# Kernel tuning notes

Hardware: AMD Instinct MI355X
Metric: run time of the kernel (lower is better)

Reference implementation:

```python
import jax, jax.numpy as jnp
import numpy as np

EPS = 1e-5
NUM_HEADS = 8

def layernorm(x, g, b):
    m = x.mean(-1, keepdims=True)
    v = ((x - m) ** 2).mean(-1, keepdims=True)
    return (x - m) / jnp.sqrt(v + EPS) * g + b

def mha(x, qkv_w, qkv_b, proj_w, proj_b):
    # x: [B, N, C]; weights stored [in, out] (transposed torch Linear)
    B, N, C = x.shape
    hd = C // NUM_HEADS
    scale = hd ** -0.5
    qkv = (x @ qkv_w + qkv_b).reshape(B, N, 3, NUM_HEADS, hd)
    qkv = jnp.transpose(qkv, (2, 0, 3, 1, 4))  # [3, B, H, N, hd]
    q, k, v = qkv[0], qkv[1], qkv[2]
    attn = jax.nn.softmax(jnp.einsum('bhnd,bhmd->bhnm', q, k) * scale, axis=-1)
    o = jnp.einsum('bhnm,bhmd->bhnd', attn, v)
    o = jnp.transpose(o, (0, 2, 1, 3)).reshape(B, N, C)
    return o @ proj_w + proj_b

def gelu(x):
    return jax.nn.gelu(x, approximate=False)

def setup_inputs() -> dict:
    key = jax.random.key(0)
    C, H = 512, 2048
    B, P, NI = 2, 196, 16
    N = 1 + NI * P
    ks = jax.random.split(key, 16)
    s = 0.02
    d = {
        'x': jax.random.normal(ks[0], (B, N, C), jnp.float32),
        'num_patches_per_image': P,
        'ln1_g': jnp.ones((C,)), 'ln1_b': jnp.zeros((C,)),
        'ln2_g': jnp.ones((C,)), 'ln2_b': jnp.zeros((C,)),
        'ln3_g': jnp.ones((C,)), 'ln3_b': jnp.zeros((C,)),
        'g_qkv_w': jax.random.normal(ks[1], (C, 3 * C)) * s,
        'g_qkv_b': jnp.zeros((3 * C,)),
        'g_proj_w': jax.random.normal(ks[2], (C, C)) * s,
        'g_proj_b': jnp.zeros((C,)),
        'l_qkv_w': jax.random.normal(ks[3], (C, 3 * C)) * s,
        'l_qkv_b': jnp.zeros((3 * C,)),
        'l_proj_w': jax.random.normal(ks[4], (C, C)) * s,
        'l_proj_b': jnp.zeros((C,)),
        'mlp_w1': jax.random.normal(ks[5], (C, H)) * s,
        'mlp_b1': jnp.zeros((H,)),
        'mlp_w2': jax.random.normal(ks[6], (H, C)) * s,
        'mlp_b2': jnp.zeros((C,)),
    }
    return d

def reference(x, num_patches_per_image, ln1_g, ln1_b, ln2_g, ln2_b, ln3_g, ln3_b,
              g_qkv_w, g_qkv_b, g_proj_w, g_proj_b,
              l_qkv_w, l_qkv_b, l_proj_w, l_proj_b,
              mlp_w1, mlp_b1, mlp_w2, mlp_b2):
    B, N, C = x.shape
    P = int(num_patches_per_image)
    NI = (N - 1) // P
    # global attention over all tokens (incl. CLS)
    x = x + mha(layernorm(x, ln1_g, ln1_b), g_qkv_w, g_qkv_b, g_proj_w, g_proj_b)
    cls_tok = x[:, 0:1, :]
    patches = x[:, 1:, :]
    # local attention: block-diagonal per-image mask == independent attention
    # within each image block (masked entries underflow to exactly 0 in softmax)
    pn = layernorm(patches, ln2_g, ln2_b).reshape(B * NI, P, C)
    local = mha(pn, l_qkv_w, l_qkv_b, l_proj_w, l_proj_b).reshape(B, NI * P, C)
    patches = patches + local
    x = jnp.concatenate([cls_tok, patches], axis=1)
    h = layernorm(x, ln3_g, ln3_b)
    h = gelu(h @ mlp_w1 + mlp_b1) @ mlp_w2 + mlp_b2
    return x + h
```

## Files before the change

### kernel.cpp

```cpp
#include <hip/hip_runtime.h>
#include <math.h>

typedef __attribute__((ext_vector_type(8))) short bf16x8;
typedef __attribute__((ext_vector_type(4))) short bf16x4_t;
typedef __attribute__((ext_vector_type(4))) float f32x4;
typedef __attribute__((ext_vector_type(4))) unsigned int u32x4;

typedef const __attribute__((address_space(1))) unsigned int glb_u32;
typedef __attribute__((address_space(3))) unsigned int lds_u32;
#define GLOAD_LDS16(g, l) __builtin_amdgcn_global_load_lds( \
    (glb_u32*)(const void*)(g), (lds_u32*)(void*)(l), 16, 0, 0)

static __device__ __forceinline__ float4 ld4(const float* p) {
    return *reinterpret_cast<const float4*>(p);
}
static __device__ __forceinline__ unsigned short f2bf(float f) {
    unsigned int u = __float_as_uint(f);
    u += 0x7fffu + ((u >> 16) & 1u);
    return (unsigned short)(u >> 16);
}

__global__ __launch_bounds__(64) void ln_kernel(
    const float* __restrict__ in, const float* __restrict__ g,
    const float* __restrict__ bta, unsigned short* __restrict__ out, int mode)
{
    int r = blockIdx.x;
    int lane = threadIdx.x;
    int in_r = mode ? (r + 1 + r / 3136) : r;
    const float* xp = in + (size_t)in_r * 512 + lane * 8;
    float4 v0 = ld4(xp), v1 = ld4(xp + 4);
    float s  = v0.x + v0.y + v0.z + v0.w + v1.x + v1.y + v1.z + v1.w;
    float sq = v0.x*v0.x + v0.y*v0.y + v0.z*v0.z + v0.w*v0.w
             + v1.x*v1.x + v1.y*v1.y + v1.z*v1.z + v1.w*v1.w;
    #pragma unroll
    for (int off = 32; off; off >>= 1) {
        s  += __shfl_xor(s, off);
        sq += __shfl_xor(sq, off);
    }
    float mean = s * (1.f / 512.f);
    float var  = fmaxf(sq * (1.f / 512.f) - mean * mean, 0.f);
    float rstd = rsqrtf(var + 1e-5f);
    float4 g0 = ld4(g + lane * 8),   g1 = ld4(g + lane * 8 + 4);
    float4 b0 = ld4(bta + lane * 8), b1 = ld4(bta + lane * 8 + 4);
    float o0 = (v0.x - mean) * rstd * g0.x + b0.x;
    float o1 = (v0.y - mean) * rstd * g0.y + b0.y;
    float o2 = (v0.z - mean) * rstd * g0.z + b0.z;
    float o3 = (v0.w - mean) * rstd * g0.w + b0.w;
    float o4 = (v1.x - mean) * rstd * g1.x + b1.x;
    float o5 = (v1.y - mean) * rstd * g1.y + b1.y;
    float o6 = (v1.z - mean) * rstd * g1.z + b1.z;
    float o7 = (v1.w - mean) * rstd * g1.w + b1.w;
    u32x4 pk;
    pk[0] = (unsigned int)f2bf(o0) | ((unsigned int)f2bf(o1) << 16);
    pk[1] = (unsigned int)f2bf(o2) | ((unsigned int)f2bf(o3) << 16);
    pk[2] = (unsigned int)f2bf(o4) | ((unsigned int)f2bf(o5) << 16);
    pk[3] = (unsigned int)f2bf(o6) | ((unsigned int)f2bf(o7) << 16);
    *(u32x4*)(out + (size_t)r * 512 + lane * 8) = pk;
}

struct TransArgs {
    const float* src[6];
    unsigned short* dst[6];
    int N[6], K[6], off[6];
};

__global__ __launch_bounds__(256) void transpose_all(TransArgs a)
{
    __shared__ unsigned short tile[32][34];
    int t = blockIdx.x;
    int i = 0;
    #pragma unroll
    for (int j = 1; j < 6; ++j) if (t >= a.off[j]) i = j;
    int rel = t - a.off[i];
    int tx_n = a.N[i] >> 5;
    int bx = (rel % tx_n) * 32, by = (rel / tx_n) * 32;
    const float* W = a.src[i];
    unsigned short* WT = a.dst[i];
    int K = a.K[i], N = a.N[i];
    int tx = threadIdx.x & 31, ty = threadIdx.x >> 5;
    #pragma unroll
    for (int r = 0; r < 32; r += 8)
        tile[ty + r][tx] = f2bf(W[(size_t)(by + ty + r) * N + bx + tx]);
    __syncthreads();
    #pragma unroll
    for (int r = 0; r < 32; r += 8)
        WT[(size_t)(bx + ty + r) * K + by + tx] = tile[tx][ty + r];
}

template<int BM, int BN, int OUT_BF16>
__global__ __launch_bounds__(256) void mfma_gemm(
    const unsigned short* __restrict__ A, const unsigned short* __restrict__ WT,
    const float* __restrict__ bias, const float* __restrict__ resid,
    void* __restrict__ outp, int M, int N, int K,
    int rowmap, int act,
    unsigned short* __restrict__ vt_out,
    int vtNs, unsigned int vtMagic, int vtNsP, int vtColBase)
{
    constexpr int FI = BM / 32, FJ = BN / 32;
    constexpr int AL = BM / 64, BL = BN / 64;
    __shared__ __align__(16) unsigned short As[2][BM * 32];
    __shared__ __align__(16) unsigned short Bs[2][BN * 32];

    int tid = threadIdx.x;
    int m0 = blockIdx.x * BM, n0 = blockIdx.y * BN;
    int w = tid >> 6, l = tid & 63;
    int wm = (w >> 1) * (BM / 2), wn = (w & 1) * (BN / 2);
    int lr = l & 15, lg = l >> 4;

    int lrow = l >> 2;
    int lcol = (l & 3) * 8;

    f32x4 zero = {0.f, 0.f, 0.f, 0.f};
    f32x4 acc[FI][FJ];
    #pragma unroll
    for (int i = 0; i < FI; ++i)
        #pragma unroll
        for (int j = 0; j < FJ; ++j) acc[i][j] = zero;

#define STAGE(buf, kk) do { \
    _Pragma("unroll") \
    for (int q = 0; q < AL; ++q) { \
        int rb = (w * AL + q) * 16; \
        GLOAD_LDS16(A + (size_t)(m0 + rb + lrow) * K + (kk) + lcol, \
                    &As[buf][rb * 32]); \
    } \
    _Pragma("unroll") \
    for (int q = 0; q < BL; ++q) { \
        int rb = (w * BL + q) * 16; \
        GLOAD_LDS16(WT + (size_t)(n0 + rb + lrow) * K + (kk) + lcol, \
                    &Bs[buf][rb * 32]); \
    } \
} while (0)

    int nk = K >> 5;
    STAGE(0, 0);
    STAGE(1, 32);
    for (int s = 0; s < nk; ++s) {
        int cur = s & 1;
        if (s + 1 < nk) {
            if constexpr (AL + BL == 2)
                asm volatile("s_waitcnt vmcnt(2)" ::: "memory");
            else if constexpr (AL + BL == 3)
                asm volatile("s_waitcnt vmcnt(3)" ::: "memory");
            else
                asm volatile("s_waitcnt vmcnt(4)" ::: "memory");
        } else {
            asm volatile("s_waitcnt vmcnt(0)" ::: "memory");
        }
        __builtin_amdgcn_s_barrier();

        bf16x8 af[FI], bfr[FJ];
        #pragma unroll
        for (int i = 0; i < FI; ++i)
            af[i] = *(const bf16x8*)&As[cur][(wm + i * 16 + lr) * 32 + lg * 8];
        #pragma unroll
        for (int j = 0; j < FJ; ++j)
            bfr[j] = *(const bf16x8*)&Bs[cur][(wn + j * 16 + lr) * 32 + lg * 8];
        asm volatile("s_waitcnt lgkmcnt(0)" ::: "memory");
        __builtin_amdgcn_sched_barrier(0);
        __builtin_amdgcn_s_barrier();
        if (s + 2 < nk) STAGE(cur, (s + 2) * 32);

        #pragma unroll
        for (int i = 0; i < FI; ++i)
            #pragma unroll
            for (int j = 0; j < FJ; ++j)
                acc[i][j] = __builtin_amdgcn_mfma_f32_16x16x32_bf16(
                    af[i], bfr[j], acc[i][j], 0, 0, 0);
    }
#undef STAGE

    int rowW = vt_out ? vtColBase : N;
    #pragma unroll
    for (int i = 0; i < FI; ++i) {
        #pragma unroll
        for (int r = 0; r < 4; ++r) {
            int row = m0 + wm + i * 16 + lg * 4 + r;
            if (row >= M) continue;
            int orow = rowmap ? (row + 1 + row / 3136) : row;
            #pragma unroll
            for (int j = 0; j < FJ; ++j) {
                int col = n0 + wn + j * 16 + lr;
                if (col >= N) continue;
                float v = acc[i][j][r] + bias[col];
                if (act) v = 0.5f * v * (1.f + erff(v * 0.70710678118654752f));
                if (resid) v += resid[(size_t)orow * N + col];
                if (vt_out && col >= vtColBase) {
                    unsigned int bb = (unsigned int)(((unsigned long long)(unsigned int)row * vtMagic) >> 32);
                    int nn = row - (int)bb * vtNs;
                    vt_out[((size_t)bb * 512 + (col - vtColBase)) * vtNsP + nn] = f2bf(v);
                } else if (OUT_BF16) {
                    ((unsigned short*)outp)[(size_t)orow * rowW + col] = f2bf(v);
                } else {
                    ((float*)outp)[(size_t)orow * rowW + col] = v;
                }
            }
        }
    }
}

__global__ __launch_bounds__(256) void attn_mfma(
    const unsigned short* __restrict__ qk, const unsigned short* __restrict__ vT,
    unsigned short* __restrict__ o, int Ns, int NsP)
{
    __shared__ __align__(16) unsigned short Ks[64 * 64];
    __shared__ __align__(16) unsigned short VsT[64 * 72];

    int tid = threadIdx.x;
    int h = blockIdx.y, b = blockIdx.z;
    int mb = b * Ns;
    int l = tid & 63, w = tid >> 6;
    int g = l >> 4, c16 = l & 15;

    int qrow = blockIdx.x * 64 + w * 16 + c16;
    int qr = (qrow < Ns ? qrow : Ns - 1) + mb;
    const unsigned short* qp = qk + (size_t)qr * 1024 + h * 64;
    bf16x8 bQ0 = *(const bf16x8*)(qp + g * 8);
    bf16x8 bQ1 = *(const bf16x8*)(qp + 32 + g * 8);

    f32x4 zero = {0.f, 0.f, 0.f, 0.f};
    f32x4 Oacc[4] = {zero, zero, zero, zero};
    float mrun = -1e30f, lrun = 0.f;

    int sk = tid >> 2, sc0 = tid & 3;
    int kswz = (sk & 7) ^ (sk >> 3);
    int kdst0 = sk * 64 + ((sc0 ^ kswz) * 8);
    int kdst1 = sk * 64 + (((sc0 + 4) ^ kswz) * 8);
    int vdst0 = sk * 72 + sc0 * 8;
    int vdst1 = sk * 72 + (sc0 + 4) * 8;
    const unsigned short* kbase = qk + (size_t)mb * 1024 + 512 + h * 64;
    const unsigned short* vrow = vT + ((size_t)b * 512 + h * 64 + sk) * NsP;

    int ka[4][2];
    #pragma unroll
    for (int f = 0; f < 4; ++f) {
        int key = 16 * f + c16;
        int swz = (key & 7) ^ (key >> 3);
        ka[f][0] = key * 64 + ((g ^ swz) * 8);
        ka[f][1] = key * 64 + (((4 + g) ^ swz) * 8);
    }

    const float SCL = 0.125f * 1.4426950408889634f;
    int nt = (Ns + 63) >> 6;
    int tail = Ns & 63;

    u32x4 kv0, kv1, vv0, vv1;
    {
        int kr = sk < Ns ? sk : Ns - 1;
        const unsigned short* kp = kbase + (size_t)kr * 1024;
        kv0 = *(const u32x4*)(kp + sc0 * 8);
        kv1 = *(const u32x4*)(kp + (sc0 + 4) * 8);
        vv0 = *(const u32x4*)(vrow + sc0 * 8);
        vv1 = *(const u32x4*)(vrow + (sc0 + 4) * 8);
    }

    for (int kt = 0; kt < nt; ++kt) {
        __syncthreads();
        *(u32x4*)&Ks[kdst0] = kv0;
        *(u32x4*)&Ks[kdst1] = kv1;
        *(u32x4*)&VsT[vdst0] = vv0;
        *(u32x4*)&VsT[vdst1] = vv1;
        __syncthreads();

        if (kt + 1 < nt) {
            int kr = (kt + 1) * 64 + sk; if (kr >= Ns) kr = Ns - 1;
            const unsigned short* kp = kbase + (size_t)kr * 1024;
            kv0 = *(const u32x4*)(kp + sc0 * 8);
            kv1 = *(const u32x4*)(kp + (sc0 + 4) * 8);
            int kb = (kt + 1) * 64;
            vv0 = *(const u32x4*)(vrow + kb + sc0 * 8);
            vv1 = *(const u32x4*)(vrow + kb + (sc0 + 4) * 8);
        }

        f32x4 st[4];
        #pragma unroll
        for (int f = 0; f < 4; ++f) {
            bf16x8 a0 = *(const bf16x8*)&Ks[ka[f][0]];
            bf16x8 a1 = *(const bf16x8*)&Ks[ka[f][1]];
            f32x4 a = zero;
            a = __builtin_amdgcn_mfma_f32_16x16x32_bf16(a0, bQ0, a, 0, 0, 0);
            a = __builtin_amdgcn_mfma_f32_16x16x32_bf16(a1, bQ1, a, 0, 0, 0);
            st[f] = a;
        }

        float sv[16];
        #pragma unroll
        for (int f = 0; f < 4; ++f)
            #pragma unroll
            for (int r = 0; r < 4; ++r) sv[4 * f + r] = st[f][r];
        if (kt == nt - 1 && tail) {
            #pragma unroll
            for (int f = 0; f < 4; ++f)
                #pragma unroll
                for (int r = 0; r < 4; ++r)
                    if (16 * f + 4 * g + r >= tail) sv[4 * f + r] = -1e30f;
        }
        float mloc = sv[0];
        #pragma unroll
        for (int e = 1; e < 16; ++e) mloc = fmaxf(mloc, sv[e]);
        if (!__all(mloc - mrun <= 64.f)) {
            mloc = fmaxf(mloc, __shfl_xor(mloc, 16));
            mloc = fmaxf(mloc, __shfl_xor(mloc, 32));
            float mnew = fmaxf(mrun, mloc);
            float sc = exp2f((mrun - mnew) * SCL);
            lrun *= sc;
            #pragma unroll
            for (int j = 0; j < 4; ++j) {
                Oacc[j][0] *= sc; Oacc[j][1] *= sc;
                Oacc[j][2] *= sc; Oacc[j][3] *= sc;
            }
            mrun = mnew;
        }
        float nl = mrun * SCL;
        #pragma unroll
        for (int e = 0; e < 16; ++e) {
            sv[e] = exp2f(fmaf(sv[e], SCL, -nl));
            lrun += sv[e];
        }

        union { unsigned int u[4]; bf16x8 v; } plo, phi;
        #pragma unroll
        for (int wi = 0; wi < 4; ++wi) {
            asm("v_cvt_pk_bf16_f32 %0, %1, %2"
                : "=v"(plo.u[wi]) : "v"(sv[2 * wi]), "v"(sv[2 * wi + 1]));
            asm("v_cvt_pk_bf16_f32 %0, %1, %2"
                : "=v"(phi.u[wi]) : "v"(sv[8 + 2 * wi]), "v"(sv[8 + 2 * wi + 1]));
        }

        #pragma unroll
        for (int j = 0; j < 4; ++j) {
            int vb = (16 * j + c16) * 72 + 4 * g;
            bf16x4_t t0 = *(const bf16x4_t*)&VsT[vb];
            bf16x4_t t1 = *(const bf16x4_t*)&VsT[vb + 16];
            bf16x4_t t2 = *(const bf16x4_t*)&VsT[vb + 32];
            bf16x4_t t3 = *(const bf16x4_t*)&VsT[vb + 48];
            bf16x8 aVlo = __builtin_shufflevector(t0, t1, 0, 1, 2, 3, 4, 5, 6, 7);
            bf16x8 aVhi = __builtin_shufflevector(t2, t3, 0, 1, 2, 3, 4, 5, 6, 7);
            Oacc[j] = __builtin_amdgcn_mfma_f32_16x16x32_bf16(aVlo, plo.v, Oacc[j], 0, 0, 0);
            Oacc[j] = __builtin_amdgcn_mfma_f32_16x16x32_bf16(aVhi, phi.v, Oacc[j], 0, 0, 0);
        }
    }

    lrun += __shfl_xor(lrun, 16);
    lrun += __shfl_xor(lrun, 32);

    if (qrow < Ns) {
        float inv = 1.f / lrun;
        unsigned short* op = o + (size_t)(mb + qrow) * 512 + h * 64;
        #pragma unroll
        for (int j = 0; j < 4; ++j) {
            unsigned int u0, u1;
            asm("v_cvt_pk_bf16_f32 %0, %1, %2"
                : "=v"(u0) : "v"(Oacc[j][0] * inv), "v"(Oacc[j][1] * inv));
            asm("v_cvt_pk_bf16_f32 %0, %1, %2"
                : "=v"(u1) : "v"(Oacc[j][2] * inv), "v"(Oacc[j][3] * inv));
            uint2 stv; stv.x = u0; stv.y = u1;
            *(uint2*)(op + 16 * j + 4 * g) = stv;
        }
    }
}

extern "C" void kernel_launch(void* const* d_in, const int* in_sizes, int n_in,
                              void* d_out, int out_size, void* d_ws, size_t ws_size,
                              hipStream_t stream)
{
    const float* x       = (const float*)d_in[0];
    const float* ln1_g   = (const float*)d_in[2];
    const float* ln1_b   = (const float*)d_in[3];
    const float* ln2_g   = (const float*)d_in[4];
    const float* ln2_b   = (const float*)d_in[5];
    const float* ln3_g   = (const float*)d_in[6];
    const float* ln3_b   = (const float*)d_in[7];
    const float* g_qkv_w = (const float*)d_in[8];
    const float* g_qkv_b = (const float*)d_in[9];
    const float* g_proj_w= (const float*)d_in[10];
    const float* g_proj_b= (const float*)d_in[11];
    const float* l_qkv_w = (const float*)d_in[12];
    const float* l_qkv_b = (const float*)d_in[13];
    const float* l_proj_w= (const float*)d_in[14];
    const float* l_proj_b= (const float*)d_in[15];
    const float* mlp_w1  = (const float*)d_in[16];
    const float* mlp_b1  = (const float*)d_in[17];
    const float* mlp_w2  = (const float*)d_in[18];
    const float* mlp_b2  = (const float*)d_in[19];

    float* out = (float*)d_out;

    unsigned short* buf_a = (unsigned short*)d_ws;
    unsigned short* buf_b = buf_a + (size_t)6274 * 512;
    unsigned short* vTb   = buf_b + (size_t)6274 * 2048;
    unsigned short* wbf   = vTb + (size_t)3276800 + 64;
    unsigned short* g_qkv_t  = wbf;
    unsigned short* g_proj_t = g_qkv_t + 1536 * 512;
    unsigned short* l_qkv_t  = g_proj_t + 512 * 512;
    unsigned short* l_proj_t = l_qkv_t + 1536 * 512;
    unsigned short* w1_t     = l_proj_t + 512 * 512;
    unsigned short* w2_t     = w1_t + (size_t)2048 * 512;

    unsigned int M3137 = (unsigned int)((0x100000000ULL + 3136) / 3137);
    unsigned int M196  = (unsigned int)((0x100000000ULL + 195) / 196);

    TransArgs ta;
    ta.src[0] = g_qkv_w;  ta.dst[0] = g_qkv_t;  ta.N[0] = 1536; ta.K[0] = 512;  ta.off[0] = 0;
    ta.src[1] = g_proj_w; ta.dst[1] = g_proj_t; ta.N[1] = 512;  ta.K[1] = 512;  ta.off[1] = 768;
    ta.src[2] = l_qkv_w;  ta.dst[2] = l_qkv_t;  ta.N[2] = 1536; ta.K[2] = 512;  ta.off[2] = 1024;
    ta.src[3] = l_proj_w; ta.dst[3] = l_proj_t; ta.N[3] = 512;  ta.K[3] = 512;  ta.off[3] = 1792;
    ta.src[4] = mlp_w1;   ta.dst[4] = w1_t;     ta.N[4] = 2048; ta.K[4] = 512;  ta.off[4] = 2048;
    ta.src[5] = mlp_w2;   ta.dst[5] = w2_t;     ta.N[5] = 512;  ta.K[5] = 2048; ta.off[5] = 3072;
    transpose_all<<<4096, 256, 0, stream>>>(ta);

    ln_kernel<<<6274, 64, 0, stream>>>(x, ln1_g, ln1_b, buf_a, 0);
    mfma_gemm<128,128,1><<<dim3(50, 12), 256, 0, stream>>>(
        buf_a, g_qkv_t, g_qkv_b, nullptr, buf_b, 6274, 1536, 512, 0, 0,
        vTb, 3137, M3137, 3144, 1024);
    attn_mfma<<<dim3(50, 8, 2), 256, 0, stream>>>(buf_b, vTb, buf_a, 3137, 3144);
    mfma_gemm<64,64,0><<<dim3(99, 8), 256, 0, stream>>>(
        buf_a, g_proj_t, g_proj_b, x, out, 6274, 512, 512, 0, 0,
        nullptr, 0, 0u, 0, 0);
    ln_kernel<<<6272, 64, 0, stream>>>(out, ln2_g, ln2_b, buf_a, 1);
    mfma_gemm<128,128,1><<<dim3(49, 12), 256, 0, stream>>>(
        buf_a, l_qkv_t, l_qkv_b, nullptr, buf_b, 6272, 1536, 512, 0, 0,
        vTb, 196, M196, 200, 1024);
    attn_mfma<<<dim3(4, 8, 32), 256, 0, stream>>>(buf_b, vTb, buf_a, 196, 200);
    mfma_gemm<64,64,0><<<dim3(98, 8), 256, 0, stream>>>(
        buf_a, l_proj_t, l_proj_b, out, out, 6272, 512, 512, 1, 0,
        nullptr, 0, 0u, 0, 0);
    ln_kernel<<<6274, 64, 0, stream>>>(out, ln3_g, ln3_b, buf_a, 0);
    mfma_gemm<128,128,1><<<dim3(50, 16), 256, 0, stream>>>(
        buf_a, w1_t, mlp_b1, nullptr, buf_b, 6274, 2048, 512, 0, 1,
        nullptr, 0, 0u, 0, 0);
    mfma_gemm<64,64,0><<<dim3(99, 8), 256, 0, stream>>>(
        buf_b, w2_t, mlp_b2, out, out, 6274, 512, 2048, 0, 0,
        nullptr, 0, 0u, 0, 0);
}
```

Measured before the change: 377.3 us.

## Double-buffer K/V tiles in attention kernel with swizzled V layout

The attention kernel now keeps two LDS buffers for K and V tiles. The next tile is stored while the current one is consumed, so each iteration needs one barrier instead of two, and global loads run two tiles ahead. The V tile switches from a padded stride-72 layout to the same XOR-swizzled 64-wide layout as K, with precomputed read addresses. It also reshapes the max reduction into a tree. LDS use rises to 32KB per block, which may reduce occupancy.

```diff
diff --git a/kernel.cpp b/kernel.cpp
--- a/kernel.cpp
+++ b/kernel.cpp
@@ -203,8 +203,8 @@
     const unsigned short* __restrict__ qk, const unsigned short* __restrict__ vT,
     unsigned short* __restrict__ o, int Ns, int NsP)
 {
-    __shared__ __align__(16) unsigned short Ks[64 * 64];
-    __shared__ __align__(16) unsigned short VsT[64 * 72];
+    __shared__ __align__(16) unsigned short Ks[2][64 * 64];
+    __shared__ __align__(16) unsigned short Vs[2][64 * 64];
 
     int tid = threadIdx.x;
     int h = blockIdx.y, b = blockIdx.z;
@@ -222,14 +222,13 @@
     f32x4 Oacc[4] = {zero, zero, zero, zero};
     float mrun = -1e30f, lrun = 0.f;
 
-    int sk = tid >> 2, sc0 = tid & 3;
-    int kswz = (sk & 7) ^ (sk >> 3);
-    int kdst0 = sk * 64 + ((sc0 ^ kswz) * 8);
-    int kdst1 = sk * 64 + (((sc0 + 4) ^ kswz) * 8);
-    int vdst0 = sk * 72 + sc0 * 8;
-    int vdst1 = sk * 72 + (sc0 + 4) * 8;
-    const unsigned short* kbase = qk + (size_t)mb * 1024 + 512 + h * 64;
-    const unsigned short* vrow = vT + ((size_t)b * 512 + h * 64 + sk) * NsP;
+    int r0 = tid >> 3, ch = tid & 7;
+    int r1 = r0 + 32;
+    int kd0 = r0 * 64 + ((ch ^ ((r0 & 7) ^ (r0 >> 3))) * 8);
+    int kd1 = r1 * 64 + ((ch ^ ((r1 & 7) ^ (r1 >> 3))) * 8);
+    const unsigned short* kbase = qk + (size_t)mb * 1024 + 512 + h * 64 + ch * 8;
+    const unsigned short* vb0 = vT + ((size_t)b * 512 + h * 64 + r0) * NsP + ch * 8;
+    const unsigned short* vb1 = vT + ((size_t)b * 512 + h * 64 + r1) * NsP + ch * 8;
 
     int ka[4][2];
     #pragma unroll
@@ -239,44 +238,57 @@
         ka[f][0] = key * 64 + ((g ^ swz) * 8);
         ka[f][1] = key * 64 + (((4 + g) ^ swz) * 8);
     }
+    int va[4][4];
+    #pragma unroll
+    for (int j = 0; j < 4; ++j) {
+        int d = 16 * j + c16;
+        int sd = (d & 7) ^ (d >> 3);
+        #pragma unroll
+        for (int t = 0; t < 4; ++t) {
+            int hc = 4 * t + g;
+            va[j][t] = d * 64 + (((hc >> 1) ^ sd) * 8) + ((g & 1) * 4);
+        }
+    }
 
     const float SCL = 0.125f * 1.4426950408889634f;
     int nt = (Ns + 63) >> 6;
     int tail = Ns & 63;
 
     u32x4 kv0, kv1, vv0, vv1;
-    {
-        int kr = sk < Ns ? sk : Ns - 1;
-        const unsigned short* kp = kbase + (size_t)kr * 1024;
-        kv0 = *(const u32x4*)(kp + sc0 * 8);
-        kv1 = *(const u32x4*)(kp + (sc0 + 4) * 8);
-        vv0 = *(const u32x4*)(vrow + sc0 * 8);
-        vv1 = *(const u32x4*)(vrow + (sc0 + 4) * 8);
-    }
-
+#define LOADT(kt) do { \
+    int kr0 = (kt) * 64 + r0; if (kr0 >= Ns) kr0 = Ns - 1; \
+    int kr1 = (kt) * 64 + r1; if (kr1 >= Ns) kr1 = Ns - 1; \
+    kv0 = *(const u32x4*)(kbase + (size_t)kr0 * 1024); \
+    kv1 = *(const u32x4*)(kbase + (size_t)kr1 * 1024); \
+    vv0 = *(const u32x4*)(vb0 + (kt) * 64); \
+    vv1 = *(const u32x4*)(vb1 + (kt) * 64); \
+} while (0)
+#define STORET(buf) do { \
+    *(u32x4*)&Ks[buf][kd0] = kv0; \
+    *(u32x4*)&Ks[buf][kd1] = kv1; \
+    *(u32x4*)&Vs[buf][kd0] = vv0; \
+    *(u32x4*)&Vs[buf][kd1] = vv1; \
+} while (0)
+
+    LOADT(0);
+    STORET(0);
+    if (nt > 1) LOADT(1);
+    __syncthreads();
+
+    int cur = 0;
     for (int kt = 0; kt < nt; ++kt) {
-        __syncthreads();
-        *(u32x4*)&Ks[kdst0] = kv0;
-        *(u32x4*)&Ks[kdst1] = kv1;
-        *(u32x4*)&VsT[vdst0] = vv0;
-        *(u32x4*)&VsT[vdst1] = vv1;
-        __syncthreads();
-
         if (kt + 1 < nt) {
-            int kr = (kt + 1) * 64 + sk; if (kr >= Ns) kr = Ns - 1;
-            const unsigned short* kp = kbase + (size_t)kr * 1024;
-            kv0 = *(const u32x4*)(kp + sc0 * 8);
-            kv1 = *(const u32x4*)(kp + (sc0 + 4) * 8);
-            int kb = (kt + 1) * 64;
-            vv0 = *(const u32x4*)(vrow + kb + sc0 * 8);
-            vv1 = *(const u32x4*)(vrow + kb + (sc0 + 4) * 8);
-        }
+            STORET(cur ^ 1);
+            if (kt + 2 < nt) LOADT(kt + 2);
+        }
+        const unsigned short* Kc = &Ks[cur][0];
+        const unsigned short* Vc = &Vs[cur][0];
 
         f32x4 st[4];
         #pragma unroll
         for (int f = 0; f < 4; ++f) {
-            bf16x8 a0 = *(const bf16x8*)&Ks[ka[f][0]];
-            bf16x8 a1 = *(const bf16x8*)&Ks[ka[f][1]];
+            bf16x8 a0 = *(const bf16x8*)&Kc[ka[f][0]];
+            bf16x8 a1 = *(const bf16x8*)&Kc[ka[f][1]];
             f32x4 a = zero;
             a = __builtin_amdgcn_mfma_f32_16x16x32_bf16(a0, bQ0, a, 0, 0, 0);
             a = __builtin_amdgcn_mfma_f32_16x16x32_bf16(a1, bQ1, a, 0, 0, 0);
@@ -295,9 +307,12 @@
                 for (int r = 0; r < 4; ++r)
                     if (16 * f + 4 * g + r >= tail) sv[4 * f + r] = -1e30f;
         }
-        float mloc = sv[0];
-        #pragma unroll
-        for (int e = 1; e < 16; ++e) mloc = fmaxf(mloc, sv[e]);
+        float m01 = fmaxf(sv[0], sv[1]), m23 = fmaxf(sv[2], sv[3]);
+        float m45 = fmaxf(sv[4], sv[5]), m67 = fmaxf(sv[6], sv[7]);
+        float m89 = fmaxf(sv[8], sv[9]), mab = fmaxf(sv[10], sv[11]);
+        float mcd = fmaxf(sv[12], sv[13]), mef = fmaxf(sv[14], sv[15]);
+        float mloc = fmaxf(fmaxf(fmaxf(m01, m23), fmaxf(m45, m67)),
+                           fmaxf(fmaxf(m89, mab), fmaxf(mcd, mef)));
         if (!__all(mloc - mrun <= 64.f)) {
             mloc = fmaxf(mloc, __shfl_xor(mloc, 16));
             mloc = fmaxf(mloc, __shfl_xor(mloc, 32));
@@ -329,17 +344,21 @@
 
         #pragma unroll
         for (int j = 0; j < 4; ++j) {
-            int vb = (16 * j + c16) * 72 + 4 * g;
-            bf16x4_t t0 = *(const bf16x4_t*)&VsT[vb];
-            bf16x4_t t1 = *(const bf16x4_t*)&VsT[vb + 16];
-            bf16x4_t t2 = *(const bf16x4_t*)&VsT[vb + 32];
-            bf16x4_t t3 = *(const bf16x4_t*)&VsT[vb + 48];
+            bf16x4_t t0 = *(const bf16x4_t*)&Vc[va[j][0]];
+            bf16x4_t t1 = *(const bf16x4_t*)&Vc[va[j][1]];
+            bf16x4_t t2 = *(const bf16x4_t*)&Vc[va[j][2]];
+            bf16x4_t t3 = *(const bf16x4_t*)&Vc[va[j][3]];
             bf16x8 aVlo = __builtin_shufflevector(t0, t1, 0, 1, 2, 3, 4, 5, 6, 7);
             bf16x8 aVhi = __builtin_shufflevector(t2, t3, 0, 1, 2, 3, 4, 5, 6, 7);
             Oacc[j] = __builtin_amdgcn_mfma_f32_16x16x32_bf16(aVlo, plo.v, Oacc[j], 0, 0, 0);
             Oacc[j] = __builtin_amdgcn_mfma_f32_16x16x32_bf16(aVhi, phi.v, Oacc[j], 0, 0, 0);
         }
-    }
+
+        __syncthreads();
+        cur ^= 1;
+    }
+#undef LOADT
+#undef STORET
 
     lrun += __shfl_xor(lrun, 16);
     lrun += __shfl_xor(lrun, 32);
```

New measurement: 381.4 us. Within noise of the previous version (+1.1%).
